# Optimization experiments

Hardware: AMD Instinct MI355X
Metric: run time of the kernel (lower is better)

Reference implementation:

```python
import jax, jax.numpy as jnp
import numpy as np

N, E = 50000, 800000
IN, HID, OUT = 128, 128, 64
BN_EPS = 1e-5


def setup_inputs() -> dict:
    key = jax.random.key(0)
    ks = jax.random.split(key, 12)
    def glorot(k, shape):
        lim = float(np.sqrt(6.0 / (shape[0] + shape[1])))
        return jax.random.uniform(k, shape, jnp.float32, -lim, lim)
    return {
        "x": jax.random.normal(ks[0], (N, IN), jnp.float32),
        "edge_index": jax.random.randint(ks[1], (2, E), 0, N, jnp.int64),
        "W1": glorot(ks[2], (IN, HID)),  "b1": jnp.zeros((HID,), jnp.float32),
        "W2": glorot(ks[3], (HID, HID)), "b2": jnp.zeros((HID,), jnp.float32),
        "W3": glorot(ks[4], (HID, OUT)), "b3": jnp.zeros((OUT,), jnp.float32),
        "gamma1": jax.random.uniform(ks[5], (HID,), jnp.float32, 0.5, 1.5),
        "beta1": jax.random.normal(ks[6], (HID,), jnp.float32) * 0.1,
        "gamma2": jax.random.uniform(ks[7], (HID,), jnp.float32, 0.5, 1.5),
        "beta2": jax.random.normal(ks[8], (HID,), jnp.float32) * 0.1,
    }


def reference(x, edge_index, W1, b1, W2, b2, W3, b3, gamma1, beta1, gamma2, beta2):
    n = x.shape[0]
    loop = jnp.arange(n, dtype=edge_index.dtype)
    src = jnp.concatenate([edge_index[0], loop])  # add self-loops (PyG GCNConv)
    dst = jnp.concatenate([edge_index[1], loop])
    deg = jax.ops.segment_sum(jnp.ones_like(dst, dtype=x.dtype), dst, num_segments=n)
    dinv = jnp.where(deg > 0, deg ** -0.5, 0.0)
    norm = (dinv[src] * dinv[dst])[:, None]  # symmetric normalization per edge

    def conv(h, W, b):
        h = h @ W                                   # [N, out]
        agg = jax.ops.segment_sum(h[src] * norm, dst, num_segments=n)
        return agg + b

    def bn(h, g, b):  # training-mode BatchNorm1d (batch stats, biased var)
        m = h.mean(axis=0)
        v = h.var(axis=0)
        return (h - m) * jax.lax.rsqrt(v + BN_EPS) * g + b

    # layer 1: in==hidden so residual applies; dropout is a no-op in eval mode
    h = jax.nn.relu(bn(conv(x, W1, b1), gamma1, beta1))
    if h.shape == x.shape:
        h = h + x
    x = h
    # layer 2: hidden -> hidden, residual
    h = jax.nn.relu(bn(conv(x, W2, b2), gamma2, beta2))
    h = h + x
    x = h
    # output layer
    return conv(x, W3, b3)
```

## Files before the change

### kernel.cpp

```cpp
#include <hip/hip_runtime.h>


#define BN_EPS 1e-5f

typedef __attribute__((ext_vector_type(8))) short bf16x8;
typedef __attribute__((ext_vector_type(4))) float f32x4;

__device__ __forceinline__ float bf2f(unsigned short u) {
    unsigned v = ((unsigned)u) << 16;
    return __builtin_bit_cast(float, v);
}
__device__ __forceinline__ unsigned short f2bf(float f) {
    unsigned u = __builtin_bit_cast(unsigned, f);
    u += 0x7fffu + ((u >> 16) & 1u);
    return (unsigned short)(u >> 16);
}

__global__ __launch_bounds__(256) void k_hist_coarse(const int* __restrict__ dst,
                                                     int* __restrict__ ccnt, int e) {
    __shared__ int hist[256];
    const int t = threadIdx.x;
    hist[t] = 0;
    __syncthreads();
    const int base = blockIdx.x * 4096;
    const int end = min(base + 4096, e);
    for (int idx = base + t; idx < end; idx += 256)
        atomicAdd(&hist[dst[idx] >> 8], 1);
    __syncthreads();
    if (hist[t] > 0) atomicAdd(&ccnt[t], hist[t]);
}

__global__ void k_scan_coarse(const int* __restrict__ ccnt, int* __restrict__ cbase,
                              int* __restrict__ ccur) {
    __shared__ int buf[256];
    const int t = threadIdx.x;
    const int v = ccnt[t];
    buf[t] = v;
    __syncthreads();
    for (int off = 1; off < 256; off <<= 1) {
        int add = (t >= off) ? buf[t - off] : 0;
        __syncthreads();
        buf[t] += add;
        __syncthreads();
    }
    const int ex = buf[t] - v;
    cbase[t] = ex;
    ccur[t] = ex;
    if (t == 255) cbase[256] = buf[255];
}

__global__ __launch_bounds__(256) void k_partition(const int* __restrict__ src,
                                                   const int* __restrict__ dst,
                                                   int* __restrict__ ccur,
                                                   unsigned int* __restrict__ pairs, int e) {
    __shared__ unsigned short dl[4096], sl[4096];
    __shared__ int hist[256], basel[256], rnk[256];
    const int t = threadIdx.x;
    const int base = blockIdx.x * 4096;
    hist[t] = 0; rnk[t] = 0;
    __syncthreads();
#pragma unroll
    for (int i = 0; i < 16; ++i) {
        int idx = base + t + i * 256;
        if (idx < e) {
            int d = dst[idx];
            dl[t + i * 256] = (unsigned short)d;
            sl[t + i * 256] = (unsigned short)src[idx];
            atomicAdd(&hist[d >> 8], 1);
        }
    }
    __syncthreads();
    if (hist[t] > 0) basel[t] = atomicAdd(&ccur[t], hist[t]);
    __syncthreads();
#pragma unroll
    for (int i = 0; i < 16; ++i) {
        int idx = base + t + i * 256;
        if (idx < e) {
            int d = dl[t + i * 256];
            int bb = d >> 8;
            int r = atomicAdd(&rnk[bb], 1);
            pairs[basel[bb] + r] = (unsigned)d | ((unsigned)sl[t + i * 256] << 16);
        }
    }
}

__global__ __launch_bounds__(256) void k_fine(const unsigned int* __restrict__ pairs,
                                              const int* __restrict__ cbase,
                                              int* __restrict__ rs, int* __restrict__ eb,
                                              float* __restrict__ dinv, int n, int e) {
    __shared__ int hist[256], fbase[256], cur[256], tmp[256];
    const int t = threadIdx.x;
    const int b = blockIdx.x;
    const int lo = cbase[b], hi = cbase[b + 1];
    hist[t] = 0; cur[t] = 0;
    __syncthreads();
    for (int pos = lo + t; pos < hi; pos += 256)
        atomicAdd(&hist[pairs[pos] & 255], 1);
    __syncthreads();
    const int v = hist[t];
    tmp[t] = v;
    __syncthreads();
    for (int off = 1; off < 256; off <<= 1) {
        int add = (t >= off) ? tmp[t - off] : 0;
        __syncthreads();
        tmp[t] += add;
        __syncthreads();
    }
    fbase[t] = tmp[t] - v;
    __syncthreads();
    const int node = b * 256 + t;
    if (node < n) {
        rs[node] = lo + fbase[t];
        dinv[node] = rsqrtf((float)(hist[t] + 1));
    }
    if (b == 0 && t == 0) rs[n] = e;
    for (int pos = lo + t; pos < hi; pos += 256) {
        unsigned pr = pairs[pos];
        int local = pr & 255;
        int r = atomicAdd(&cur[local], 1);
        eb[lo + fbase[local] + r] = (int)(pr >> 16);
    }
}

__device__ __forceinline__ void packW_one(const float* __restrict__ W,
                                          unsigned short* __restrict__ Wp,
                                          int ncol, int tid) {
    const int nct = ncol >> 4;
    int lane = tid & 63;
    int f = tid >> 6;
    int ct = f % nct;
    int kc = f / nct;
    int n = ct * 16 + (lane & 15);
    int k0 = kc * 32 + (lane >> 4) * 8;
    ushort4 lo, hi;
    lo.x = f2bf(W[(size_t)(k0 + 0) * ncol + n]);
    lo.y = f2bf(W[(size_t)(k0 + 1) * ncol + n]);
    lo.z = f2bf(W[(size_t)(k0 + 2) * ncol + n]);
    lo.w = f2bf(W[(size_t)(k0 + 3) * ncol + n]);
    hi.x = f2bf(W[(size_t)(k0 + 4) * ncol + n]);
    hi.y = f2bf(W[(size_t)(k0 + 5) * ncol + n]);
    hi.z = f2bf(W[(size_t)(k0 + 6) * ncol + n]);
    hi.w = f2bf(W[(size_t)(k0 + 7) * ncol + n]);
    *(ushort4*)(Wp + (size_t)tid * 8)     = lo;
    *(ushort4*)(Wp + (size_t)tid * 8 + 4) = hi;
}

__global__ void k_packW_all(const float* __restrict__ W1, const float* __restrict__ W2,
                            const float* __restrict__ W3,
                            unsigned short* __restrict__ Wp1, unsigned short* __restrict__ Wp2,
                            unsigned short* __restrict__ Wp3) {
    int tid = blockIdx.x * 256 + threadIdx.x;
    if (tid < 2048)      packW_one(W1, Wp1, 128, tid);
    else if (tid < 4096) packW_one(W2, Wp2, 128, tid - 2048);
    else if (tid < 5120) packW_one(W3, Wp3, 64, tid - 4096);
}

__global__ __launch_bounds__(256) void k_gemm_mfma128_f32(
        const float* __restrict__ Af, const unsigned short* __restrict__ Wp,
        unsigned short* __restrict__ xs, const float* __restrict__ dinv, int n) {
    __shared__ __align__(16) unsigned short Wl[16384];
    const int t = threadIdx.x;
    {
        const ushort4* s = (const ushort4*)Wp;
        ushort4* d = (ushort4*)Wl;
#pragma unroll
        for (int i = 0; i < 16; ++i) d[t + 256 * i] = s[t + 256 * i];
    }
    __syncthreads();
    const int lane = t & 63, wave = t >> 6;
    const int quad = lane >> 4, l15 = lane & 15;
    const int m0 = blockIdx.x * 64 + wave * 16;
    const int arow = min(m0 + l15, n - 1);

    f32x4 acc[8];
#pragma unroll
    for (int ct = 0; ct < 8; ++ct) acc[ct] = (f32x4){0.f, 0.f, 0.f, 0.f};

#pragma unroll
    for (int kc = 0; kc < 4; ++kc) {
        float4 alo = *(const float4*)(Af + (size_t)arow * 128 + kc * 32 + quad * 8);
        float4 ahi = *(const float4*)(Af + (size_t)arow * 128 + kc * 32 + quad * 8 + 4);
        bf16x8 a;
        a[0] = (short)f2bf(alo.x); a[1] = (short)f2bf(alo.y);
        a[2] = (short)f2bf(alo.z); a[3] = (short)f2bf(alo.w);
        a[4] = (short)f2bf(ahi.x); a[5] = (short)f2bf(ahi.y);
        a[6] = (short)f2bf(ahi.z); a[7] = (short)f2bf(ahi.w);
#pragma unroll
        for (int ct = 0; ct < 8; ++ct) {
            bf16x8 b = *(const bf16x8*)(Wl + ((kc * 8 + ct) * 64 + lane) * 8);
            acc[ct] = __builtin_amdgcn_mfma_f32_16x16x32_bf16(a, b, acc[ct], 0, 0, 0);
        }
    }

    int rowv[4]; float dvv[4];
#pragma unroll
    for (int r = 0; r < 4; ++r) {
        rowv[r] = m0 + quad * 4 + r;
        dvv[r] = dinv[min(rowv[r], n - 1)];
    }
#pragma unroll
    for (int ct = 0; ct < 8; ++ct)
#pragma unroll
        for (int r = 0; r < 4; ++r)
            if (rowv[r] < n)
                xs[(size_t)rowv[r] * 128 + ct * 16 + l15] = f2bf(acc[ct][r] * dvv[r]);
}

__global__ __launch_bounds__(256) void k_gemm_mfma128_bn(
        const float* __restrict__ agg, const float* __restrict__ res,
        const float* __restrict__ gsum, const float* __restrict__ gsq,
        const float* __restrict__ gamma, const float* __restrict__ beta, float inv_n,
        unsigned short* __restrict__ h_out, const unsigned short* __restrict__ Wp,
        unsigned short* __restrict__ xs, const float* __restrict__ dinv, int n) {
    __shared__ __align__(16) unsigned short Wl[16384];
    __shared__ float s_sc[128], s_sh[128];
    const int t = threadIdx.x;
    {
        const ushort4* s = (const ushort4*)Wp;
        ushort4* d = (ushort4*)Wl;
#pragma unroll
        for (int i = 0; i < 16; ++i) d[t + 256 * i] = s[t + 256 * i];
    }
    if (t < 128) {
        float m = gsum[t] * inv_n;
        float v = gsq[t] * inv_n - m * m;
        float sc = gamma[t] * rsqrtf(v + BN_EPS);
        s_sc[t] = sc;
        s_sh[t] = beta[t] - m * sc;
    }
    __syncthreads();
    const int lane = t & 63, wave = t >> 6;
    const int quad = lane >> 4, l15 = lane & 15;
    const int m0 = blockIdx.x * 64 + wave * 16;
    const int arow = min(m0 + l15, n - 1);

    f32x4 acc[8];
#pragma unroll
    for (int ct = 0; ct < 8; ++ct) acc[ct] = (f32x4){0.f, 0.f, 0.f, 0.f};

#pragma unroll
    for (int kc = 0; kc < 4; ++kc) {
        const int f = kc * 32 + quad * 8;
        float4 g0 = *(const float4*)(agg + (size_t)arow * 128 + f);
        float4 g1 = *(const float4*)(agg + (size_t)arow * 128 + f + 4);
        float4 r0 = *(const float4*)(res + (size_t)arow * 128 + f);
        float4 r1 = *(const float4*)(res + (size_t)arow * 128 + f + 4);
        bf16x8 a;
        a[0] = (short)f2bf(fmaxf(fmaf(g0.x, s_sc[f + 0], s_sh[f + 0]), 0.f) + r0.x);
        a[1] = (short)f2bf(fmaxf(fmaf(g0.y, s_sc[f + 1], s_sh[f + 1]), 0.f) + r0.y);
        a[2] = (short)f2bf(fmaxf(fmaf(g0.z, s_sc[f + 2], s_sh[f + 2]), 0.f) + r0.z);
        a[3] = (short)f2bf(fmaxf(fmaf(g0.w, s_sc[f + 3], s_sh[f + 3]), 0.f) + r0.w);
        a[4] = (short)f2bf(fmaxf(fmaf(g1.x, s_sc[f + 4], s_sh[f + 4]), 0.f) + r1.x);
        a[5] = (short)f2bf(fmaxf(fmaf(g1.y, s_sc[f + 5], s_sh[f + 5]), 0.f) + r1.y);
        a[6] = (short)f2bf(fmaxf(fmaf(g1.z, s_sc[f + 6], s_sh[f + 6]), 0.f) + r1.z);
        a[7] = (short)f2bf(fmaxf(fmaf(g1.w, s_sc[f + 7], s_sh[f + 7]), 0.f) + r1.w);
        *(bf16x8*)(h_out + (size_t)arow * 128 + f) = a;
#pragma unroll
        for (int ct = 0; ct < 8; ++ct) {
            bf16x8 b = *(const bf16x8*)(Wl + ((kc * 8 + ct) * 64 + lane) * 8);
            acc[ct] = __builtin_amdgcn_mfma_f32_16x16x32_bf16(a, b, acc[ct], 0, 0, 0);
        }
    }

    int rowv[4]; float dvv[4];
#pragma unroll
    for (int r = 0; r < 4; ++r) {
        rowv[r] = m0 + quad * 4 + r;
        dvv[r] = dinv[min(rowv[r], n - 1)];
    }
#pragma unroll
    for (int ct = 0; ct < 8; ++ct)
#pragma unroll
        for (int r = 0; r < 4; ++r)
            if (rowv[r] < n)
                xs[(size_t)rowv[r] * 128 + ct * 16 + l15] = f2bf(acc[ct][r] * dvv[r]);
}

__global__ __launch_bounds__(256) void k_gemm_mfma64_bn(
        const float* __restrict__ agg, const unsigned short* __restrict__ res,
        const float* __restrict__ gsum, const float* __restrict__ gsq,
        const float* __restrict__ gamma, const float* __restrict__ beta, float inv_n,
        const unsigned short* __restrict__ Wp,
        unsigned short* __restrict__ xs, const float* __restrict__ dinv, int n) {
    __shared__ __align__(16) unsigned short Wl[8192];
    __shared__ float s_sc[128], s_sh[128];
    const int t = threadIdx.x;
    {
        const ushort4* s = (const ushort4*)Wp;
        ushort4* d = (ushort4*)Wl;
#pragma unroll
        for (int i = 0; i < 8; ++i) d[t + 256 * i] = s[t + 256 * i];
    }
    if (t < 128) {
        float m = gsum[t] * inv_n;
        float v = gsq[t] * inv_n - m * m;
        float sc = gamma[t] * rsqrtf(v + BN_EPS);
        s_sc[t] = sc;
        s_sh[t] = beta[t] - m * sc;
    }
    __syncthreads();
    const int lane = t & 63, wave = t >> 6;
    const int quad = lane >> 4, l15 = lane & 15;
    const int m0 = blockIdx.x * 64 + wave * 16;
    const int arow = min(m0 + l15, n - 1);

    f32x4 acc[4];
#pragma unroll
    for (int ct = 0; ct < 4; ++ct) acc[ct] = (f32x4){0.f, 0.f, 0.f, 0.f};

#pragma unroll
    for (int kc = 0; kc < 4; ++kc) {
        const int f = kc * 32 + quad * 8;
        float4 g0 = *(const float4*)(agg + (size_t)arow * 128 + f);
        float4 g1 = *(const float4*)(agg + (size_t)arow * 128 + f + 4);
        bf16x8 rv = *(const bf16x8*)(res + (size_t)arow * 128 + f);
        bf16x8 a;
        a[0] = (short)f2bf(fmaxf(fmaf(g0.x, s_sc[f + 0], s_sh[f + 0]), 0.f) + bf2f((unsigned short)rv[0]));
        a[1] = (short)f2bf(fmaxf(fmaf(g0.y, s_sc[f + 1], s_sh[f + 1]), 0.f) + bf2f((unsigned short)rv[1]));
        a[2] = (short)f2bf(fmaxf(fmaf(g0.z, s_sc[f + 2], s_sh[f + 2]), 0.f) + bf2f((unsigned short)rv[2]));
        a[3] = (short)f2bf(fmaxf(fmaf(g0.w, s_sc[f + 3], s_sh[f + 3]), 0.f) + bf2f((unsigned short)rv[3]));
        a[4] = (short)f2bf(fmaxf(fmaf(g1.x, s_sc[f + 4], s_sh[f + 4]), 0.f) + bf2f((unsigned short)rv[4]));
        a[5] = (short)f2bf(fmaxf(fmaf(g1.y, s_sc[f + 5], s_sh[f + 5]), 0.f) + bf2f((unsigned short)rv[5]));
        a[6] = (short)f2bf(fmaxf(fmaf(g1.z, s_sc[f + 6], s_sh[f + 6]), 0.f) + bf2f((unsigned short)rv[6]));
        a[7] = (short)f2bf(fmaxf(fmaf(g1.w, s_sc[f + 7], s_sh[f + 7]), 0.f) + bf2f((unsigned short)rv[7]));
#pragma unroll
        for (int ct = 0; ct < 4; ++ct) {
            bf16x8 b = *(const bf16x8*)(Wl + ((kc * 4 + ct) * 64 + lane) * 8);
            acc[ct] = __builtin_amdgcn_mfma_f32_16x16x32_bf16(a, b, acc[ct], 0, 0, 0);
        }
    }

    int rowv[4]; float dvv[4];
#pragma unroll
    for (int r = 0; r < 4; ++r) {
        rowv[r] = m0 + quad * 4 + r;
        dvv[r] = dinv[min(rowv[r], n - 1)];
    }
#pragma unroll
    for (int ct = 0; ct < 4; ++ct)
#pragma unroll
        for (int r = 0; r < 4; ++r)
            if (rowv[r] < n)
                xs[(size_t)rowv[r] * 64 + ct * 16 + l15] = f2bf(acc[ct][r] * dvv[r]);
}

__global__ __launch_bounds__(256) void k_gather128(
        float* __restrict__ agg, const unsigned short* __restrict__ xs,
        const int* __restrict__ rs, const int* __restrict__ eb,
        const float* __restrict__ dinv, float* __restrict__ scratch, int n) {
    const int t = threadIdx.x;
    const int lane = t & 31;
    const int node = blockIdx.x * 8 + (t >> 5);
    const ushort4* xv = (const ushort4*)xs;
    float4 o = {0.f, 0.f, 0.f, 0.f};
    if (node < n) {
        ushort4 v = xv[(size_t)node * 32 + lane];
        float ax0 = bf2f(v.x), ay0 = bf2f(v.y), az0 = bf2f(v.z), aw0 = bf2f(v.w);
        float ax1 = 0.f, ay1 = 0.f, az1 = 0.f, aw1 = 0.f;
        int b = rs[node], e = rs[node + 1];
        int i = b;
        for (; i + 4 <= e; i += 4) {
            int sA = eb[i], sB = eb[i + 1], sC = eb[i + 2], sD = eb[i + 3];
            ushort4 uA = xv[(size_t)sA * 32 + lane];
            ushort4 uB = xv[(size_t)sB * 32 + lane];
            ushort4 uC = xv[(size_t)sC * 32 + lane];
            ushort4 uD = xv[(size_t)sD * 32 + lane];
            ax0 += bf2f(uA.x); ay0 += bf2f(uA.y); az0 += bf2f(uA.z); aw0 += bf2f(uA.w);
            ax1 += bf2f(uB.x); ay1 += bf2f(uB.y); az1 += bf2f(uB.z); aw1 += bf2f(uB.w);
            ax0 += bf2f(uC.x); ay0 += bf2f(uC.y); az0 += bf2f(uC.z); aw0 += bf2f(uC.w);
            ax1 += bf2f(uD.x); ay1 += bf2f(uD.y); az1 += bf2f(uD.z); aw1 += bf2f(uD.w);
        }
        for (; i < e; ++i) {
            ushort4 u = xv[(size_t)eb[i] * 32 + lane];
            ax0 += bf2f(u.x); ay0 += bf2f(u.y); az0 += bf2f(u.z); aw0 += bf2f(u.w);
        }
        float dv = dinv[node];
        o.x = (ax0 + ax1) * dv; o.y = (ay0 + ay1) * dv;
        o.z = (az0 + az1) * dv; o.w = (aw0 + aw1) * dv;
        ((float4*)agg)[(size_t)node * 32 + lane] = o;
    }
    __shared__ float4 lsum[256], lsq[256];
    lsum[t] = o;
    lsq[t]  = (float4){o.x * o.x, o.y * o.y, o.z * o.z, o.w * o.w};
    __syncthreads();
    if (t < 32) {
        float4 a = lsum[t], b = lsq[t];
#pragma unroll
        for (int g = 1; g < 8; ++g) {
            float4 u = lsum[t + 32 * g], w = lsq[t + 32 * g];
            a.x += u.x; a.y += u.y; a.z += u.z; a.w += u.w;
            b.x += w.x; b.y += w.y; b.z += w.z; b.w += w.w;
        }
        ((float4*)scratch)[(size_t)blockIdx.x * 64 + t]      = a;
        ((float4*)scratch)[(size_t)blockIdx.x * 64 + 32 + t] = b;
    }
}

__global__ __launch_bounds__(256) void k_colreduce(const float* __restrict__ scratch,
                                                   float* __restrict__ gsum,
                                                   float* __restrict__ gsq, int nblk) {
    const int c = blockIdx.x;
    const int t = threadIdx.x;
    float s = 0.f, q = 0.f;
    for (int b = t; b < nblk; b += 256) {
        s += scratch[(size_t)b * 256 + c];
        q += scratch[(size_t)b * 256 + 128 + c];
    }
    __shared__ float ls[256], lq[256];
    ls[t] = s; lq[t] = q;
    __syncthreads();
    for (int off = 128; off; off >>= 1) {
        if (t < off) { ls[t] += ls[t + off]; lq[t] += lq[t + off]; }
        __syncthreads();
    }
    if (t == 0) { gsum[c] = ls[0]; gsq[c] = lq[0]; }
}

__global__ void k_gather64_bias(float* __restrict__ out, const unsigned short* __restrict__ xs,
                                const int* __restrict__ rs, const int* __restrict__ eb,
                                const float* __restrict__ dinv, const float* __restrict__ bias,
                                int n) {
    int node = blockIdx.x * 16 + (threadIdx.x >> 4);
    int lane = threadIdx.x & 15;
    if (node >= n) return;
    const ushort4* xv = (const ushort4*)xs;
    ushort4 v = xv[(size_t)node * 16 + lane];
    float ax0 = bf2f(v.x), ay0 = bf2f(v.y), az0 = bf2f(v.z), aw0 = bf2f(v.w);
    float ax1 = 0.f, ay1 = 0.f, az1 = 0.f, aw1 = 0.f;
    int b = rs[node], e = rs[node + 1];
    int i = b;
    for (; i + 4 <= e; i += 4) {
        int sA = eb[i], sB = eb[i + 1], sC = eb[i + 2], sD = eb[i + 3];
        ushort4 uA = xv[(size_t)sA * 16 + lane];
        ushort4 uB = xv[(size_t)sB * 16 + lane];
        ushort4 uC = xv[(size_t)sC * 16 + lane];
        ushort4 uD = xv[(size_t)sD * 16 + lane];
        ax0 += bf2f(uA.x); ay0 += bf2f(uA.y); az0 += bf2f(uA.z); aw0 += bf2f(uA.w);
        ax1 += bf2f(uB.x); ay1 += bf2f(uB.y); az1 += bf2f(uB.z); aw1 += bf2f(uB.w);
        ax0 += bf2f(uC.x); ay0 += bf2f(uC.y); az0 += bf2f(uC.z); aw0 += bf2f(uC.w);
        ax1 += bf2f(uD.x); ay1 += bf2f(uD.y); az1 += bf2f(uD.z); aw1 += bf2f(uD.w);
    }
    for (; i < e; ++i) {
        ushort4 u = xv[(size_t)eb[i] * 16 + lane];
        ax0 += bf2f(u.x); ay0 += bf2f(u.y); az0 += bf2f(u.z); aw0 += bf2f(u.w);
    }
    float dv = dinv[node];
    const float4* bv = (const float4*)bias;
    float4 bb = bv[lane];
    float4 o;
    o.x = (ax0 + ax1) * dv + bb.x; o.y = (ay0 + ay1) * dv + bb.y;
    o.z = (az0 + az1) * dv + bb.z; o.w = (aw0 + aw1) * dv + bb.w;
    ((float4*)out)[(size_t)node * 16 + lane] = o;
}

extern "C" void kernel_launch(void* const* d_in, const int* in_sizes, int n_in,
                              void* d_out, int out_size, void* d_ws, size_t ws_size,
                              hipStream_t stream) {
    const float* x   = (const float*)d_in[0];
    const int*   ei  = (const int*)d_in[1];
    const float* W1  = (const float*)d_in[2];
    const float* W2  = (const float*)d_in[4];
    const float* W3  = (const float*)d_in[6];
    const float* b3  = (const float*)d_in[7];
    const float* g1  = (const float*)d_in[8];
    const float* be1 = (const float*)d_in[9];
    const float* g2  = (const float*)d_in[10];
    const float* be2 = (const float*)d_in[11];
    float* out = (float*)d_out;

    const int N = in_sizes[0] / 128;
    const int E = in_sizes[1] / 2;
    const int* src = ei;
    const int* dst = ei + E;

    const int gG = (N + 7) / 8;

    char* p = (char*)d_ws;
    float* dinv  = (float*)p;               p += (size_t)N * 4;
    unsigned short* xs = (unsigned short*)p; p += (size_t)N * 128 * 2;
    unsigned short* h1 = (unsigned short*)p; p += (size_t)N * 128 * 2;
    float* agg   = (float*)p;               p += (size_t)N * 128 * 4;
    float* gsum  = (float*)p;               p += 128 * 4;
    float* gsq   = (float*)p;               p += 128 * 4;
    float* scratch = (float*)p;             p += (size_t)gG * 256 * 4;
    unsigned short* Wp1 = (unsigned short*)p; p += 16384 * 2;
    unsigned short* Wp2 = (unsigned short*)p; p += 16384 * 2;
    unsigned short* Wp3 = (unsigned short*)p; p += 8192 * 2;
    int*   ccnt  = (int*)p;                 p += 256 * 4;
    int*   cbase = (int*)p;                 p += 260 * 4;
    int*   ccur  = (int*)p;                 p += 256 * 4;
    unsigned int* pairs = (unsigned int*)p; p += (size_t)E * 4;
    int*   rs    = (int*)p;                 p += (size_t)(N + 16) * 4;
    int*   eb    = (int*)p;                 p += (size_t)E * 4;

    const int B = 256;
    const int gT    = (N + 63) / 64;
    const int gEchk = (E + 4095) / 4096;
    const int gN256 = (N + 255) / 256;
    const float inv_n = 1.0f / (float)N;

    hipMemsetAsync(ccnt, 0, 256 * 4, stream);
    k_hist_coarse<<<gEchk, B, 0, stream>>>(dst, ccnt, E);
    k_scan_coarse<<<1, B, 0, stream>>>(ccnt, cbase, ccur);
    k_partition<<<gEchk, B, 0, stream>>>(src, dst, ccur, pairs, E);
    k_fine<<<gN256, B, 0, stream>>>(pairs, cbase, rs, eb, dinv, N, E);
    k_packW_all<<<20, B, 0, stream>>>(W1, W2, W3, Wp1, Wp2, Wp3);

    k_gemm_mfma128_f32<<<gT, B, 0, stream>>>(x, Wp1, xs, dinv, N);
    k_gather128<<<gG, B, 0, stream>>>(agg, xs, rs, eb, dinv, scratch, N);
    k_colreduce<<<128, B, 0, stream>>>(scratch, gsum, gsq, gG);

    k_gemm_mfma128_bn<<<gT, B, 0, stream>>>(agg, x, gsum, gsq, g1, be1, inv_n,
                                            h1, Wp2, xs, dinv, N);
    k_gather128<<<gG, B, 0, stream>>>(agg, xs, rs, eb, dinv, scratch, N);
    k_colreduce<<<128, B, 0, stream>>>(scratch, gsum, gsq, gG);

    k_gemm_mfma64_bn<<<gT, B, 0, stream>>>(agg, h1, gsum, gsq, g2, be2, inv_n,
                                           Wp3, xs, dinv, N);
    k_gather64_bias<<<(N + 15) / 16, B, 0, stream>>>(out, xs, rs, eb, dinv, b3, N);
}
```

Baseline: 317.1 us.

## Store aggregates in bf16, fuse weight packing into histogram, unroll gathers deeper

The intermediate aggregation buffer is now stored as bf16 instead of fp32, which halves its write traffic in the gather kernels and its read traffic in the following GEMM+BN kernels. The coarse histogram now writes per-chunk counts that the scan kernel sums, so the global atomics and the memset go away. Weight packing is folded into that same launch, removing a separate kernel. The gather loops are unrolled from 4 to 8 edges to keep more loads in flight. Column statistics are still computed from the fp32 values, but the BN input is now rounded to bf16, which adds some precision loss.

```diff
diff --git a/kernel.cpp b/kernel.cpp
--- a/kernel.cpp
+++ b/kernel.cpp
@@ -14,112 +14,6 @@
     unsigned u = __builtin_bit_cast(unsigned, f);
     u += 0x7fffu + ((u >> 16) & 1u);
     return (unsigned short)(u >> 16);
-}
-
-__global__ __launch_bounds__(256) void k_hist_coarse(const int* __restrict__ dst,
-                                                     int* __restrict__ ccnt, int e) {
-    __shared__ int hist[256];
-    const int t = threadIdx.x;
-    hist[t] = 0;
-    __syncthreads();
-    const int base = blockIdx.x * 4096;
-    const int end = min(base + 4096, e);
-    for (int idx = base + t; idx < end; idx += 256)
-        atomicAdd(&hist[dst[idx] >> 8], 1);
-    __syncthreads();
-    if (hist[t] > 0) atomicAdd(&ccnt[t], hist[t]);
-}
-
-__global__ void k_scan_coarse(const int* __restrict__ ccnt, int* __restrict__ cbase,
-                              int* __restrict__ ccur) {
-    __shared__ int buf[256];
-    const int t = threadIdx.x;
-    const int v = ccnt[t];
-    buf[t] = v;
-    __syncthreads();
-    for (int off = 1; off < 256; off <<= 1) {
-        int add = (t >= off) ? buf[t - off] : 0;
-        __syncthreads();
-        buf[t] += add;
-        __syncthreads();
-    }
-    const int ex = buf[t] - v;
-    cbase[t] = ex;
-    ccur[t] = ex;
-    if (t == 255) cbase[256] = buf[255];
-}
-
-__global__ __launch_bounds__(256) void k_partition(const int* __restrict__ src,
-                                                   const int* __restrict__ dst,
-                                                   int* __restrict__ ccur,
-                                                   unsigned int* __restrict__ pairs, int e) {
-    __shared__ unsigned short dl[4096], sl[4096];
-    __shared__ int hist[256], basel[256], rnk[256];
-    const int t = threadIdx.x;
-    const int base = blockIdx.x * 4096;
-    hist[t] = 0; rnk[t] = 0;
-    __syncthreads();
-#pragma unroll
-    for (int i = 0; i < 16; ++i) {
-        int idx = base + t + i * 256;
-        if (idx < e) {
-            int d = dst[idx];
-            dl[t + i * 256] = (unsigned short)d;
-            sl[t + i * 256] = (unsigned short)src[idx];
-            atomicAdd(&hist[d >> 8], 1);
-        }
-    }
-    __syncthreads();
-    if (hist[t] > 0) basel[t] = atomicAdd(&ccur[t], hist[t]);
-    __syncthreads();
-#pragma unroll
-    for (int i = 0; i < 16; ++i) {
-        int idx = base + t + i * 256;
-        if (idx < e) {
-            int d = dl[t + i * 256];
-            int bb = d >> 8;
-            int r = atomicAdd(&rnk[bb], 1);
-            pairs[basel[bb] + r] = (unsigned)d | ((unsigned)sl[t + i * 256] << 16);
-        }
-    }
-}
-
-__global__ __launch_bounds__(256) void k_fine(const unsigned int* __restrict__ pairs,
-                                              const int* __restrict__ cbase,
-                                              int* __restrict__ rs, int* __restrict__ eb,
-                                              float* __restrict__ dinv, int n, int e) {
-    __shared__ int hist[256], fbase[256], cur[256], tmp[256];
-    const int t = threadIdx.x;
-    const int b = blockIdx.x;
-    const int lo = cbase[b], hi = cbase[b + 1];
-    hist[t] = 0; cur[t] = 0;
-    __syncthreads();
-    for (int pos = lo + t; pos < hi; pos += 256)
-        atomicAdd(&hist[pairs[pos] & 255], 1);
-    __syncthreads();
-    const int v = hist[t];
-    tmp[t] = v;
-    __syncthreads();
-    for (int off = 1; off < 256; off <<= 1) {
-        int add = (t >= off) ? tmp[t - off] : 0;
-        __syncthreads();
-        tmp[t] += add;
-        __syncthreads();
-    }
-    fbase[t] = tmp[t] - v;
-    __syncthreads();
-    const int node = b * 256 + t;
-    if (node < n) {
-        rs[node] = lo + fbase[t];
-        dinv[node] = rsqrtf((float)(hist[t] + 1));
-    }
-    if (b == 0 && t == 0) rs[n] = e;
-    for (int pos = lo + t; pos < hi; pos += 256) {
-        unsigned pr = pairs[pos];
-        int local = pr & 255;
-        int r = atomicAdd(&cur[local], 1);
-        eb[lo + fbase[local] + r] = (int)(pr >> 16);
-    }
 }
 
 __device__ __forceinline__ void packW_one(const float* __restrict__ W,
@@ -145,14 +39,119 @@
     *(ushort4*)(Wp + (size_t)tid * 8 + 4) = hi;
 }
 
-__global__ void k_packW_all(const float* __restrict__ W1, const float* __restrict__ W2,
-                            const float* __restrict__ W3,
-                            unsigned short* __restrict__ Wp1, unsigned short* __restrict__ Wp2,
-                            unsigned short* __restrict__ Wp3) {
-    int tid = blockIdx.x * 256 + threadIdx.x;
+__global__ __launch_bounds__(256) void k_hist_pack(
+        const int* __restrict__ dst, int* __restrict__ chist, int e,
+        const float* __restrict__ W1, const float* __restrict__ W2,
+        const float* __restrict__ W3,
+        unsigned short* __restrict__ Wp1, unsigned short* __restrict__ Wp2,
+        unsigned short* __restrict__ Wp3) {
+    __shared__ int hist[256];
+    const int t = threadIdx.x;
+    hist[t] = 0;
+    __syncthreads();
+    const int base = blockIdx.x * 4096;
+    const int end = min(base + 4096, e);
+    for (int idx = base + t; idx < end; idx += 256)
+        atomicAdd(&hist[dst[idx] >> 8], 1);
+    __syncthreads();
+    chist[blockIdx.x * 256 + t] = hist[t];
+    int tid = blockIdx.x * 256 + t;
     if (tid < 2048)      packW_one(W1, Wp1, 128, tid);
     else if (tid < 4096) packW_one(W2, Wp2, 128, tid - 2048);
     else if (tid < 5120) packW_one(W3, Wp3, 64, tid - 4096);
+}
+
+__global__ void k_scan_coarse(const int* __restrict__ chist, int nchunk,
+                              int* __restrict__ cbase, int* __restrict__ ccur) {
+    __shared__ int buf[256];
+    const int t = threadIdx.x;
+    int v = 0;
+    for (int c = 0; c < nchunk; ++c) v += chist[c * 256 + t];
+    buf[t] = v;
+    __syncthreads();
+    for (int off = 1; off < 256; off <<= 1) {
+        int add = (t >= off) ? buf[t - off] : 0;
+        __syncthreads();
+        buf[t] += add;
+        __syncthreads();
+    }
+    const int ex = buf[t] - v;
+    cbase[t] = ex;
+    ccur[t] = ex;
+    if (t == 255) cbase[256] = buf[255];
+}
+
+__global__ __launch_bounds__(256) void k_partition(const int* __restrict__ src,
+                                                   const int* __restrict__ dst,
+                                                   int* __restrict__ ccur,
+                                                   unsigned int* __restrict__ pairs, int e) {
+    __shared__ unsigned short dl[4096], sl[4096];
+    __shared__ int hist[256], basel[256], rnk[256];
+    const int t = threadIdx.x;
+    const int base = blockIdx.x * 4096;
+    hist[t] = 0; rnk[t] = 0;
+    __syncthreads();
+#pragma unroll
+    for (int i = 0; i < 16; ++i) {
+        int idx = base + t + i * 256;
+        if (idx < e) {
+            int d = dst[idx];
+            dl[t + i * 256] = (unsigned short)d;
+            sl[t + i * 256] = (unsigned short)src[idx];
+            atomicAdd(&hist[d >> 8], 1);
+        }
+    }
+    __syncthreads();
+    if (hist[t] > 0) basel[t] = atomicAdd(&ccur[t], hist[t]);
+    __syncthreads();
+#pragma unroll
+    for (int i = 0; i < 16; ++i) {
+        int idx = base + t + i * 256;
+        if (idx < e) {
+            int d = dl[t + i * 256];
+            int bb = d >> 8;
+            int r = atomicAdd(&rnk[bb], 1);
+            pairs[basel[bb] + r] = (unsigned)d | ((unsigned)sl[t + i * 256] << 16);
+        }
+    }
+}
+
+__global__ __launch_bounds__(256) void k_fine(const unsigned int* __restrict__ pairs,
+                                              const int* __restrict__ cbase,
+                                              int* __restrict__ rs, int* __restrict__ eb,
+                                              float* __restrict__ dinv, int n, int e) {
+    __shared__ int hist[256], fbase[256], cur[256], tmp[256];
+    const int t = threadIdx.x;
+    const int b = blockIdx.x;
+    const int lo = cbase[b], hi = cbase[b + 1];
+    hist[t] = 0; cur[t] = 0;
+    __syncthreads();
+    for (int pos = lo + t; pos < hi; pos += 256)
+        atomicAdd(&hist[pairs[pos] & 255], 1);
+    __syncthreads();
+    const int v = hist[t];
+    tmp[t] = v;
+    __syncthreads();
+    for (int off = 1; off < 256; off <<= 1) {
+        int add = (t >= off) ? tmp[t - off] : 0;
+        __syncthreads();
+        tmp[t] += add;
+        __syncthreads();
+    }
+    fbase[t] = tmp[t] - v;
+    __syncthreads();
+    const int node = b * 256 + t;
+    if (node < n) {
+        rs[node] = lo + fbase[t];
+        dinv[node] = rsqrtf((float)(hist[t] + 1));
+    }
+    if (b == 0 && t == 0) rs[n] = e;
+    for (int pos = lo + t; pos < hi; pos += 256) {
+        unsigned pr = pairs[pos];
+        int local = pr & 255;
+        int r = atomicAdd(&cur[local], 1);
+        eb[lo + fbase[local] + r] = (int)(pr >> 16);
+    }
 }
 
 __global__ __launch_bounds__(256) void k_gemm_mfma128_f32(
@@ -207,7 +206,7 @@
 }
 
 __global__ __launch_bounds__(256) void k_gemm_mfma128_bn(
-        const float* __restrict__ agg, const float* __restrict__ res,
+        const unsigned short* __restrict__ agg, const float* __restrict__ res,
         const float* __restrict__ gsum, const float* __restrict__ gsq,
         const float* __restrict__ gamma, const float* __restrict__ beta, float inv_n,
         unsigned short* __restrict__ h_out, const unsigned short* __restrict__ Wp,
@@ -241,19 +240,18 @@
 #pragma unroll
     for (int kc = 0; kc < 4; ++kc) {
         const int f = kc * 32 + quad * 8;
-        float4 g0 = *(const float4*)(agg + (size_t)arow * 128 + f);
-        float4 g1 = *(const float4*)(agg + (size_t)arow * 128 + f + 4);
+        bf16x8 gv = *(const bf16x8*)(agg + (size_t)arow * 128 + f);
         float4 r0 = *(const float4*)(res + (size_t)arow * 128 + f);
         float4 r1 = *(const float4*)(res + (size_t)arow * 128 + f + 4);
         bf16x8 a;
-        a[0] = (short)f2bf(fmaxf(fmaf(g0.x, s_sc[f + 0], s_sh[f + 0]), 0.f) + r0.x);
-        a[1] = (short)f2bf(fmaxf(fmaf(g0.y, s_sc[f + 1], s_sh[f + 1]), 0.f) + r0.y);
-        a[2] = (short)f2bf(fmaxf(fmaf(g0.z, s_sc[f + 2], s_sh[f + 2]), 0.f) + r0.z);
-        a[3] = (short)f2bf(fmaxf(fmaf(g0.w, s_sc[f + 3], s_sh[f + 3]), 0.f) + r0.w);
-        a[4] = (short)f2bf(fmaxf(fmaf(g1.x, s_sc[f + 4], s_sh[f + 4]), 0.f) + r1.x);
-        a[5] = (short)f2bf(fmaxf(fmaf(g1.y, s_sc[f + 5], s_sh[f + 5]), 0.f) + r1.y);
-        a[6] = (short)f2bf(fmaxf(fmaf(g1.z, s_sc[f + 6], s_sh[f + 6]), 0.f) + r1.z);
-        a[7] = (short)f2bf(fmaxf(fmaf(g1.w, s_sc[f + 7], s_sh[f + 7]), 0.f) + r1.w);
+        a[0] = (short)f2bf(fmaxf(fmaf(bf2f((unsigned short)gv[0]), s_sc[f + 0], s_sh[f + 0]), 0.f) + r0.x);
+        a[1] = (short)f2bf(fmaxf(fmaf(bf2f((unsigned short)gv[1]), s_sc[f + 1], s_sh[f + 1]), 0.f) + r0.y);
+        a[2] = (short)f2bf(fmaxf(fmaf(bf2f((unsigned short)gv[2]), s_sc[f + 2], s_sh[f + 2]), 0.f) + r0.z);
+        a[3] = (short)f2bf(fmaxf(fmaf(bf2f((unsigned short)gv[3]), s_sc[f + 3], s_sh[f + 3]), 0.f) + r0.w);
+        a[4] = (short)f2bf(fmaxf(fmaf(bf2f((unsigned short)gv[4]), s_sc[f + 4], s_sh[f + 4]), 0.f) + r1.x);
+        a[5] = (short)f2bf(fmaxf(fmaf(bf2f((unsigned short)gv[5]), s_sc[f + 5], s_sh[f + 5]), 0.f) + r1.y);
+        a[6] = (short)f2bf(fmaxf(fmaf(bf2f((unsigned short)gv[6]), s_sc[f + 6], s_sh[f + 6]), 0.f) + r1.z);
+        a[7] = (short)f2bf(fmaxf(fmaf(bf2f((unsigned short)gv[7]), s_sc[f + 7], s_sh[f + 7]), 0.f) + r1.w);
         *(bf16x8*)(h_out + (size_t)arow * 128 + f) = a;
 #pragma unroll
         for (int ct = 0; ct < 8; ++ct) {
@@ -277,7 +275,7 @@
 }
 
 __global__ __launch_bounds__(256) void k_gemm_mfma64_bn(
-        const float* __restrict__ agg, const unsigned short* __restrict__ res,
+        const unsigned short* __restrict__ agg, const unsigned short* __restrict__ res,
         const float* __restrict__ gsum, const float* __restrict__ gsq,
         const float* __restrict__ gamma, const float* __restrict__ beta, float inv_n,
         const unsigned short* __restrict__ Wp,
@@ -311,18 +309,13 @@
 #pragma unroll
     for (int kc = 0; kc < 4; ++kc) {
         const int f = kc * 32 + quad * 8;
-        float4 g0 = *(const float4*)(agg + (size_t)arow * 128 + f);
-        float4 g1 = *(const float4*)(agg + (size_t)arow * 128 + f + 4);
+        bf16x8 gv = *(const bf16x8*)(agg + (size_t)arow * 128 + f);
         bf16x8 rv = *(const bf16x8*)(res + (size_t)arow * 128 + f);
         bf16x8 a;
-        a[0] = (short)f2bf(fmaxf(fmaf(g0.x, s_sc[f + 0], s_sh[f + 0]), 0.f) + bf2f((unsigned short)rv[0]));
-        a[1] = (short)f2bf(fmaxf(fmaf(g0.y, s_sc[f + 1], s_sh[f + 1]), 0.f) + bf2f((unsigned short)rv[1]));
-        a[2] = (short)f2bf(fmaxf(fmaf(g0.z, s_sc[f + 2], s_sh[f + 2]), 0.f) + bf2f((unsigned short)rv[2]));
-        a[3] = (short)f2bf(fmaxf(fmaf(g0.w, s_sc[f + 3], s_sh[f + 3]), 0.f) + bf2f((unsigned short)rv[3]));
-        a[4] = (short)f2bf(fmaxf(fmaf(g1.x, s_sc[f + 4], s_sh[f + 4]), 0.f) + bf2f((unsigned short)rv[4]));
-        a[5] = (short)f2bf(fmaxf(fmaf(g1.y, s_sc[f + 5], s_sh[f + 5]), 0.f) + bf2f((unsigned short)rv[5]));
-        a[6] = (short)f2bf(fmaxf(fmaf(g1.z, s_sc[f + 6], s_sh[f + 6]), 0.f) + bf2f((unsigned short)rv[6]));
-        a[7] = (short)f2bf(fmaxf(fmaf(g1.w, s_sc[f + 7], s_sh[f + 7]), 0.f) + bf2f((unsigned short)rv[7]));
+#pragma unroll
+        for (int j = 0; j < 8; ++j)
+            a[j] = (short)f2bf(fmaxf(fmaf(bf2f((unsigned short)gv[j]), s_sc[f + j], s_sh[f + j]), 0.f)
+                               + bf2f((unsigned short)rv[j]));
 #pragma unroll
         for (int ct = 0; ct < 4; ++ct) {
             bf16x8 b = *(const bf16x8*)(Wl + ((kc * 4 + ct) * 64 + lane) * 8);
@@ -345,7 +338,7 @@
 }
 
 __global__ __launch_bounds__(256) void k_gather128(
-        float* __restrict__ agg, const unsigned short* __restrict__ xs,
+        unsigned short* __restrict__ agg, const unsigned short* __restrict__ xs,
         const int* __restrict__ rs, const int* __restrict__ eb,
         const float* __restrict__ dinv, float* __restrict__ scratch, int n) {
     const int t = threadIdx.x;
@@ -359,25 +352,42 @@
         float ax1 = 0.f, ay1 = 0.f, az1 = 0.f, aw1 = 0.f;
         int b = rs[node], e = rs[node + 1];
         int i = b;
-        for (; i + 4 <= e; i += 4) {
-            int sA = eb[i], sB = eb[i + 1], sC = eb[i + 2], sD = eb[i + 3];
-            ushort4 uA = xv[(size_t)sA * 32 + lane];
-            ushort4 uB = xv[(size_t)sB * 32 + lane];
-            ushort4 uC = xv[(size_t)sC * 32 + lane];
-            ushort4 uD = xv[(size_t)sD * 32 + lane];
-            ax0 += bf2f(uA.x); ay0 += bf2f(uA.y); az0 += bf2f(uA.z); aw0 += bf2f(uA.w);
-            ax1 += bf2f(uB.x); ay1 += bf2f(uB.y); az1 += bf2f(uB.z); aw1 += bf2f(uB.w);
-            ax0 += bf2f(uC.x); ay0 += bf2f(uC.y); az0 += bf2f(uC.z); aw0 += bf2f(uC.w);
-            ax1 += bf2f(uD.x); ay1 += bf2f(uD.y); az1 += bf2f(uD.z); aw1 += bf2f(uD.w);
-        }
-        for (; i < e; ++i) {
+        for (; i + 8 <= e; i += 8) {
+            int s0 = eb[i],     s1 = eb[i + 1], s2 = eb[i + 2], s3 = eb[i + 3];
+            int s4 = eb[i + 4], s5 = eb[i + 5], s6 = eb[i + 6], s7 = eb[i + 7];
+            ushort4 u0 = xv[(size_t)s0 * 32 + lane];
+            ushort4 u1 = xv[(size_t)s1 * 32 + lane];
+            ushort4 u2 = xv[(size_t)s2 * 32 + lane];
+            ushort4 u3 = xv[(size_t)s3 * 32 + lane];
+            ushort4 u4 = xv[(size_t)s4 * 32 + lane];
+            ushort4 u5 = xv[(size_t)s5 * 32 + lane];
+            ushort4 u6 = xv[(size_t)s6 * 32 + lane];
+            ushort4 u7 = xv[(size_t)s7 * 32 + lane];
+            ax0 += bf2f(u0.x); ay0 += bf2f(u0.y); az0 += bf2f(u0.z); aw0 += bf2f(u0.w);
+            ax1 += bf2f(u1.x); ay1 += bf2f(u1.y); az1 += bf2f(u1.z); aw1 += bf2f(u1.w);
+            ax0 += bf2f(u2.x); ay0 += bf2f(u2.y); az0 += bf2f(u2.z); aw0 += bf2f(u2.w);
+            ax1 += bf2f(u3.x); ay1 += bf2f(u3.y); az1 += bf2f(u3.z); aw1 += bf2f(u3.w);
+            ax0 += bf2f(u4.x); ay0 += bf2f(u4.y); az0 += bf2f(u4.z); aw0 += bf2f(u4.w);
+            ax1 += bf2f(u5.x); ay1 += bf2f(u5.y); az1 += bf2f(u5.z); aw1 += bf2f(u5.w);
+            ax0 += bf2f(u6.x); ay0 += bf2f(u6.y); az0 += bf2f(u6.z); aw0 += bf2f(u6.w);
+            ax1 += bf2f(u7.x); ay1 += bf2f(u7.y); az1 += bf2f(u7.z); aw1 += bf2f(u7.w);
+        }
+        for (; i + 2 <= e; i += 2) {
+            int s0 = eb[i], s1 = eb[i + 1];
+            ushort4 u0 = xv[(size_t)s0 * 32 + lane];
+            ushort4 u1 = xv[(size_t)s1 * 32 + lane];
+            ax0 += bf2f(u0.x); ay0 += bf2f(u0.y); az0 += bf2f(u0.z); aw0 += bf2f(u0.w);
+            ax1 += bf2f(u1.x); ay1 += bf2f(u1.y); az1 += bf2f(u1.z); aw1 += bf2f(u1.w);
+        }
+        if (i < e) {
             ushort4 u = xv[(size_t)eb[i] * 32 + lane];
             ax0 += bf2f(u.x); ay0 += bf2f(u.y); az0 += bf2f(u.z); aw0 += bf2f(u.w);
         }
         float dv = dinv[node];
         o.x = (ax0 + ax1) * dv; o.y = (ay0 + ay1) * dv;
         o.z = (az0 + az1) * dv; o.w = (aw0 + aw1) * dv;
-        ((float4*)agg)[(size_t)node * 32 + lane] = o;
+        ushort4 ob = { f2bf(o.x), f2bf(o.y), f2bf(o.z), f2bf(o.w) };
+        ((ushort4*)agg)[(size_t)node * 32 + lane] = ob;
     }
     __shared__ float4 lsum[256], lsq[256];
     lsum[t] = o;
@@ -429,18 +439,34 @@
     float ax1 = 0.f, ay1 = 0.f, az1 = 0.f, aw1 = 0.f;
     int b = rs[node], e = rs[node + 1];
     int i = b;
-    for (; i + 4 <= e; i += 4) {
-        int sA = eb[i], sB = eb[i + 1], sC = eb[i + 2], sD = eb[i + 3];
-        ushort4 uA = xv[(size_t)sA * 16 + lane];
-        ushort4 uB = xv[(size_t)sB * 16 + lane];
-        ushort4 uC = xv[(size_t)sC * 16 + lane];
-        ushort4 uD = xv[(size_t)sD * 16 + lane];
-        ax0 += bf2f(uA.x); ay0 += bf2f(uA.y); az0 += bf2f(uA.z); aw0 += bf2f(uA.w);
-        ax1 += bf2f(uB.x); ay1 += bf2f(uB.y); az1 += bf2f(uB.z); aw1 += bf2f(uB.w);
-        ax0 += bf2f(uC.x); ay0 += bf2f(uC.y); az0 += bf2f(uC.z); aw0 += bf2f(uC.w);
-        ax1 += bf2f(uD.x); ay1 += bf2f(uD.y); az1 += bf2f(uD.z); aw1 += bf2f(uD.w);
-    }
-    for (; i < e; ++i) {
+    for (; i + 8 <= e; i += 8) {
+        int s0 = eb[i],     s1 = eb[i + 1], s2 = eb[i + 2], s3 = eb[i + 3];
+        int s4 = eb[i + 4], s5 = eb[i + 5], s6 = eb[i + 6], s7 = eb[i + 7];
+        ushort4 u0 = xv[(size_t)s0 * 16 + lane];
+        ushort4 u1 = xv[(size_t)s1 * 16 + lane];
+        ushort4 u2 = xv[(size_t)s2 * 16 + lane];
+        ushort4 u3 = xv[(size_t)s3 * 16 + lane];
+        ushort4 u4 = xv[(size_t)s4 * 16 + lane];
+        ushort4 u5 = xv[(size_t)s5 * 16 + lane];
+        ushort4 u6 = xv[(size_t)s6 * 16 + lane];
+        ushort4 u7 = xv[(size_t)s7 * 16 + lane];
+        ax0 += bf2f(u0.x); ay0 += bf2f(u0.y); az0 += bf2f(u0.z); aw0 += bf2f(u0.w);
+        ax1 += bf2f(u1.x); ay1 += bf2f(u1.y); az1 += bf2f(u1.z); aw1 += bf2f(u1.w);
+        ax0 += bf2f(u2.x); ay0 += bf2f(u2.y); az0 += bf2f(u2.z); aw0 += bf2f(u2.w);
+        ax1 += bf2f(u3.x); ay1 += bf2f(u3.y); az1 += bf2f(u3.z); aw1 += bf2f(u3.w);
+        ax0 += bf2f(u4.x); ay0 += bf2f(u4.y); az0 += bf2f(u4.z); aw0 += bf2f(u4.w);
+        ax1 += bf2f(u5.x); ay1 += bf2f(u5.y); az1 += bf2f(u5.z); aw1 += bf2f(u5.w);
+        ax0 += bf2f(u6.x); ay0 += bf2f(u6.y); az0 += bf2f(u6.z); aw0 += bf2f(u6.w);
+        ax1 += bf2f(u7.x); ay1 += bf2f(u7.y); az1 += bf2f(u7.z); aw1 += bf2f(u7.w);
+    }
+    for (; i + 2 <= e; i += 2) {
+        int s0 = eb[i], s1 = eb[i + 1];
+        ushort4 u0 = xv[(size_t)s0 * 16 + lane];
+        ushort4 u1 = xv[(size_t)s1 * 16 + lane];
+        ax0 += bf2f(u0.x); ay0 += bf2f(u0.y); az0 += bf2f(u0.z); aw0 += bf2f(u0.w);
+        ax1 += bf2f(u1.x); ay1 += bf2f(u1.y); az1 += bf2f(u1.z); aw1 += bf2f(u1.w);
+    }
+    if (i < e) {
         ushort4 u = xv[(size_t)eb[i] * 16 + lane];
         ax0 += bf2f(u.x); ay0 += bf2f(u.y); az0 += bf2f(u.z); aw0 += bf2f(u.w);
     }
@@ -473,20 +499,21 @@
     const int* src = ei;
     const int* dst = ei + E;
 
-    const int gG = (N + 7) / 8;
+    const int gG    = (N + 7) / 8;
+    const int gEchk = (E + 4095) / 4096;
 
     char* p = (char*)d_ws;
     float* dinv  = (float*)p;               p += (size_t)N * 4;
     unsigned short* xs = (unsigned short*)p; p += (size_t)N * 128 * 2;
     unsigned short* h1 = (unsigned short*)p; p += (size_t)N * 128 * 2;
-    float* agg   = (float*)p;               p += (size_t)N * 128 * 4;
+    unsigned short* agg = (unsigned short*)p; p += (size_t)N * 128 * 2;
     float* gsum  = (float*)p;               p += 128 * 4;
     float* gsq   = (float*)p;               p += 128 * 4;
     float* scratch = (float*)p;             p += (size_t)gG * 256 * 4;
     unsigned short* Wp1 = (unsigned short*)p; p += 16384 * 2;
     unsigned short* Wp2 = (unsigned short*)p; p += 16384 * 2;
     unsigned short* Wp3 = (unsigned short*)p; p += 8192 * 2;
-    int*   ccnt  = (int*)p;                 p += 256 * 4;
+    int*   chist = (int*)p;                 p += (size_t)gEchk * 256 * 4;
     int*   cbase = (int*)p;                 p += 260 * 4;
     int*   ccur  = (int*)p;                 p += 256 * 4;
     unsigned int* pairs = (unsigned int*)p; p += (size_t)E * 4;
@@ -495,16 +522,13 @@
 
     const int B = 256;
     const int gT    = (N + 63) / 64;
-    const int gEchk = (E + 4095) / 4096;
     const int gN256 = (N + 255) / 256;
     const float inv_n = 1.0f / (float)N;
 
-    hipMemsetAsync(ccnt, 0, 256 * 4, stream);
-    k_hist_coarse<<<gEchk, B, 0, stream>>>(dst, ccnt, E);
-    k_scan_coarse<<<1, B, 0, stream>>>(ccnt, cbase, ccur);
+    k_hist_pack<<<gEchk, B, 0, stream>>>(dst, chist, E, W1, W2, W3, Wp1, Wp2, Wp3);
+    k_scan_coarse<<<1, B, 0, stream>>>(chist, gEchk, cbase, ccur);
     k_partition<<<gEchk, B, 0, stream>>>(src, dst, ccur, pairs, E);
     k_fine<<<gN256, B, 0, stream>>>(pairs, cbase, rs, eb, dinv, N, E);
-    k_packW_all<<<20, B, 0, stream>>>(W1, W2, W3, Wp1, Wp2, Wp3);
 
     k_gemm_mfma128_f32<<<gT, B, 0, stream>>>(x, Wp1, xs, dinv, N);
     k_gather128<<<gG, B, 0, stream>>>(agg, xs, rs, eb, dinv, scratch, N);
```

Result: no change. 323.3 us (+2.0%).
